# Kernel tuning notes

Hardware: AMD Instinct MI355X
Metric: run time of the kernel (lower is better)

## Reference

```python
import math
import jax, jax.numpy as jnp
import numpy as np

D_MODEL = 96
D_INNER = 192   # ssm_ratio * d_model
D_STATE = 16
DT_RANK = 6     # ceil(96/16)
B_, L_ = 4, 4096
LN_EPS = 1e-5


def selective_scan(u, delta, A, Bm, Cm, D):
    """Mamba selective scan (selective_scan_fn_v1 semantics).
    u, delta: [b,d,l]; A: [d,n]; Bm, Cm: [b,n,l]; D: [d]. Returns [b,d,l]."""
    b, d, l = u.shape
    n = A.shape[1]
    dT = jnp.transpose(delta, (2, 0, 1))  # [l,b,d]
    uT = jnp.transpose(u, (2, 0, 1))      # [l,b,d]
    BT = jnp.transpose(Bm, (2, 0, 1))     # [l,b,n]
    CT = jnp.transpose(Cm, (2, 0, 1))     # [l,b,n]

    def step(h, xs):
        dt, ut, Bt, Ct = xs
        dA = jnp.exp(dt[:, :, None] * A[None, :, :])            # [b,d,n]
        h = dA * h + (dt * ut)[:, :, None] * Bt[:, None, :]     # [b,d,n]
        y = jnp.sum(h * Ct[:, None, :], axis=-1)                # [b,d]
        return h, y

    h0 = jnp.zeros((b, d, n), u.dtype)
    _, ys = jax.lax.scan(step, h0, (dT, uT, BT, CT))            # ys: [l,b,d]
    return jnp.transpose(ys, (1, 2, 0)) + D[:, None] * u


def layer_norm(x, g, b):
    mu = jnp.mean(x, axis=-1, keepdims=True)
    var = jnp.var(x, axis=-1, keepdims=True)
    return (x - mu) * jax.lax.rsqrt(var + LN_EPS) * g + b


def branch_proj(x_bld, Wx, Wdt, bdt):
    """x_bld: [b,l,d_inner] -> delta [b,d,l], B [b,n,l], C [b,n,l]."""
    x_dbl = jnp.einsum('bld,kd->blk', x_bld, Wx)                # [b,l,r+2n]
    dt_r = x_dbl[..., :DT_RANK]
    Bm = jnp.transpose(x_dbl[..., DT_RANK:DT_RANK + D_STATE], (0, 2, 1))
    Cm = jnp.transpose(x_dbl[..., DT_RANK + D_STATE:], (0, 2, 1))
    dt = jnp.einsum('blr,dr->bdl', dt_r, Wdt)                   # [b,d,l]
    delta = jax.nn.softplus(dt + bdt[None, :, None])
    return delta, Bm, Cm


def forward_impl(x_rgb, x_share_rgb, x_e, x_share_e,
                 Wx1, Wx2, Wxs, Wdt1, Wdt2, Wdts, bdt1, bdt2, bdts,
                 Alog1, Alog2, Alogs, D1, D2, Ds,
                 g1, be1, g2, be2, gs, bes):
    u_rgb = jnp.transpose(x_rgb, (0, 2, 1))     # [b,d,l]
    u_e = jnp.transpose(x_e, (0, 2, 1))
    x_share = x_share_rgb + x_share_e           # [b,l,d]

    d_rgb, B_rgb, C_rgb = branch_proj(x_rgb, Wx1, Wdt1, bdt1)
    d_e, B_e, C_e = branch_proj(x_e, Wx2, Wdt2, bdt2)
    d_sh, B_sh, C_sh = branch_proj(x_share, Wxs, Wdts, bdts)

    A1 = -jnp.exp(Alog1)
    A2 = -jnp.exp(Alog2)
    As = -jnp.exp(Alogs)

    # Cross=True: rgb branch uses C from e branch, and vice versa
    y_rgb = selective_scan(u_rgb, d_rgb, A1, B_rgb, C_e, D1)
    y_e = selective_scan(u_e, d_e, A2, B_e, C_rgb, D2)
    y_sh_rgb = selective_scan(u_rgb, d_sh, As, B_sh, C_sh, Ds)
    y_sh_e = selective_scan(u_e, d_sh, As, B_sh, C_sh, Ds)

    y_rgb = layer_norm(jnp.transpose(y_rgb, (0, 2, 1)), g1, be1)
    y_e = layer_norm(jnp.transpose(y_e, (0, 2, 1)), g2, be2)
    y_sh_rgb = layer_norm(jnp.transpose(y_sh_rgb, (0, 2, 1)), gs, bes)
    y_sh_e = layer_norm(jnp.transpose(y_sh_e, (0, 2, 1)), gs, bes)
    return (y_rgb, y_sh_rgb, y_e, y_sh_e)


def setup_inputs() -> dict:
    key = jax.random.key(0)
    ks = jax.random.split(key, 16)
    inp = {}
    inp['x_rgb'] = jax.random.normal(ks[0], (B_, L_, D_INNER), jnp.float32)
    inp['x_share_rgb'] = jax.random.normal(ks[1], (B_, L_, D_INNER), jnp.float32)
    inp['x_e'] = jax.random.normal(ks[2], (B_, L_, D_INNER), jnp.float32)
    inp['x_share_e'] = jax.random.normal(ks[3], (B_, L_, D_INNER), jnp.float32)

    kproj = DT_RANK + 2 * D_STATE
    std = 1.0 / math.sqrt(D_INNER)
    inp['Wx1'] = jax.random.uniform(ks[4], (kproj, D_INNER), jnp.float32, -std, std)
    inp['Wx2'] = jax.random.uniform(ks[5], (kproj, D_INNER), jnp.float32, -std, std)
    inp['Wxs'] = jax.random.uniform(ks[6], (kproj, D_INNER), jnp.float32, -std, std)

    dt_std = DT_RANK ** -0.5
    inp['Wdt1'] = jax.random.uniform(ks[7], (D_INNER, DT_RANK), jnp.float32, -dt_std, dt_std)
    inp['Wdt2'] = jax.random.uniform(ks[8], (D_INNER, DT_RANK), jnp.float32, -dt_std, dt_std)
    inp['Wdts'] = jax.random.uniform(ks[9], (D_INNER, DT_RANK), jnp.float32, -dt_std, dt_std)

    def dt_bias(k):
        dt = jnp.exp(jax.random.uniform(k, (D_INNER,)) * (math.log(0.1) - math.log(0.001)) + math.log(0.001))
        dt = jnp.clip(dt, 1e-4, None)
        return dt + jnp.log(-jnp.expm1(-dt))  # inverse softplus
    inp['bdt1'] = dt_bias(ks[10])
    inp['bdt2'] = dt_bias(ks[11])
    inp['bdts'] = dt_bias(ks[12])

    Alog = jnp.log(jnp.broadcast_to(jnp.arange(1, D_STATE + 1, dtype=jnp.float32), (D_INNER, D_STATE)))
    inp['Alog1'] = Alog; inp['Alog2'] = Alog; inp['Alogs'] = Alog
    inp['D1'] = jnp.ones((D_INNER,), jnp.float32)
    inp['D2'] = jnp.ones((D_INNER,), jnp.float32)
    inp['Ds'] = jnp.ones((D_INNER,), jnp.float32)
    for nm in ('g1', 'g2', 'gs'):
        inp[nm] = jnp.ones((D_INNER,), jnp.float32)
    for nm in ('be1', 'be2', 'bes'):
        inp[nm] = jnp.zeros((D_INNER,), jnp.float32)
    return inp


def reference(x_rgb, x_share_rgb, x_e, x_share_e,
              Wx1, Wx2, Wxs, Wdt1, Wdt2, Wdts, bdt1, bdt2, bdts,
              Alog1, Alog2, Alogs, D1, D2, Ds,
              g1, be1, g2, be2, gs, bes):
    return forward_impl(x_rgb, x_share_rgb, x_e, x_share_e,
                        Wx1, Wx2, Wxs, Wdt1, Wdt2, Wdts, bdt1, bdt2, bdts,
                        Alog1, Alog2, Alogs, D1, D2, Ds,
                        g1, be1, g2, be2, gs, bes)
```

## Files before the change

kernel.cpp:

```cpp
#include <hip/hip_runtime.h>

#define B_ 4
#define L_ 4096
#define D_ 192
#define N_ 16
#define K_ 38
#define BLD (B_*L_*D_)
#define LOG2E 1.44269504088896f

__device__ __forceinline__ float fexp2(float x){ return __builtin_amdgcn_exp2f(x); }

__device__ __forceinline__ float softplus_f(float z){
    return fmaxf(z, 0.f) + __logf(1.f + __expf(-fabsf(z)));
}

__global__ __launch_bounds__(256) void proj_kernel(
    const float* __restrict__ xr,  const float* __restrict__ xsr,
    const float* __restrict__ xe,  const float* __restrict__ xse,
    const float* __restrict__ Wx1, const float* __restrict__ Wx2,
    const float* __restrict__ Wxs, float* __restrict__ xdbl)
{
    __shared__ float4 Wl[K_ * 48];
    __shared__ float4 xs[24 * 64];

    int branch = blockIdx.x >> 8;
    int tile   = blockIdx.x & 255;
    int tid  = threadIdx.x;
    int lane = tid & 63;
    int wv   = tid >> 6;

    const float* W = (branch == 0 ? Wx1 : branch == 1 ? Wx2 : Wxs);
    const float4* Wg = (const float4*)W;
    #pragma unroll
    for (int i = 0; i < 8; i++){
        int idx = tid + i * 256;
        if (idx < K_ * 48) Wl[idx] = Wg[idx];
    }

    const float* xA;
    const float* xB = nullptr;
    if (branch == 0)      xA = xr;
    else if (branch == 1) xA = xe;
    else { xA = xsr; xB = xse; }

    int c0 = wv * 10;
    int ncols = (wv < 3) ? 10 : 8;

    float acc[10];
    #pragma unroll
    for (int j = 0; j < 10; j++) acc[j] = 0.f;

    #pragma unroll
    for (int p = 0; p < 2; p++){
        __syncthreads();
        #pragma unroll
        for (int i = 0; i < 6; i++){
            int f4 = i * 256 + tid;
            int r  = f4 / 24;
            int kl = f4 - r * 24;
            const float4* src = (const float4*)(xA + (size_t)(tile * 64 + r) * D_);
            float4 v = src[p * 24 + kl];
            if (branch == 2){
                const float4* srcb = (const float4*)(xB + (size_t)(tile * 64 + r) * D_);
                float4 t = srcb[p * 24 + kl];
                v.x += t.x; v.y += t.y; v.z += t.z; v.w += t.w;
            }
            xs[kl * 64 + ((r + kl) & 63)] = v;
        }
        __syncthreads();
        #pragma unroll 4
        for (int kl = 0; kl < 24; kl++){
            float4 xv = xs[kl * 64 + ((lane + kl) & 63)];
            int k4 = p * 24 + kl;
            #pragma unroll
            for (int j = 0; j < 10; j++){
                if (j < ncols){
                    float4 wv4 = Wl[(c0 + j) * 48 + k4];
                    acc[j] = fmaf(xv.x, wv4.x, fmaf(xv.y, wv4.y,
                             fmaf(xv.z, wv4.z, fmaf(xv.w, wv4.w, acc[j]))));
                }
            }
        }
    }

    int gr = branch * (B_ * L_) + tile * 64 + lane;
    float* o = xdbl + (size_t)gr * K_ + c0;
    #pragma unroll
    for (int j = 0; j < 10; j++)
        if (j < ncols) o[j] = acc[j];
}

template<int NCt>
__global__ __launch_bounds__(192) void passA_kernel(
    const float* __restrict__ xdbl,
    const float* __restrict__ xr, const float* __restrict__ xe,
    const float* __restrict__ Wdt1, const float* __restrict__ Wdt2, const float* __restrict__ Wdts,
    const float* __restrict__ bdt1, const float* __restrict__ bdt2, const float* __restrict__ bdts,
    const float* __restrict__ Alog1, const float* __restrict__ Alog2, const float* __restrict__ Alogs,
    float* __restrict__ Sbuf, float* __restrict__ dsum)
{
    constexpr int CHt = L_ / NCt;
    int blk = blockIdx.x;
    int job = blk / (B_ * NCt);
    int rem = blk - job * (B_ * NCt);
    int b = rem / NCt;
    int c = rem - b * NCt;
    int d = threadIdx.x;
    const bool shared = (job == 2);

    const float* Wdt  = job == 0 ? Wdt1  : job == 1 ? Wdt2  : Wdts;
    const float* bdtp = job == 0 ? bdt1  : job == 1 ? bdt2  : bdts;
    const float* Alog = job == 0 ? Alog1 : job == 1 ? Alog2 : Alogs;

    float w[6];
    #pragma unroll
    for (int r = 0; r < 6; r++) w[r] = Wdt[d * 6 + r];
    float bd = bdtp[d];
    float A2[N_];
    #pragma unroll
    for (int n = 0; n < N_; n++) A2[n] = -__expf(Alog[d * N_ + n]) * LOG2E;

    float h[N_], h2[N_];
    #pragma unroll
    for (int n = 0; n < N_; n++){ h[n] = 0.f; h2[n] = 0.f; }
    float ds = 0.f;

    const float* u1 = (job == 1) ? xe : xr;
    const float* row = xdbl + ((size_t)(job * B_ + b) * L_ + (size_t)c * CHt) * K_;
    size_t uoff = ((size_t)b * L_ + (size_t)c * CHt) * D_ + d;

    float cur[22];
    #pragma unroll
    for (int i = 0; i < 22; i++) cur[i] = row[i];
    float uv  = u1[uoff];
    float uv2 = shared ? xe[uoff] : 0.f;

    for (int s = 0; s < CHt; s++){
        float nxt[22];
        #pragma unroll
        for (int i = 0; i < 22; i++) nxt[i] = row[K_ + i];
        size_t uoff_n = uoff + (s + 1 < CHt ? (size_t)D_ : 0);
        float uv_n  = u1[uoff_n];
        float uv2_n = shared ? xe[uoff_n] : 0.f;

        float z = bd;
        #pragma unroll
        for (int r = 0; r < 6; r++) z = fmaf(cur[r], w[r], z);
        float delta = softplus_f(z);
        ds += delta;
        float du  = delta * uv;
        float du2 = delta * uv2;
        #pragma unroll
        for (int n = 0; n < N_; n++){
            float dA = fexp2(delta * A2[n]);
            float bn = cur[6 + n];
            h[n] = fmaf(dA, h[n], du * bn);
            if (shared) h2[n] = fmaf(dA, h2[n], du2 * bn);
        }
        row += K_;
        #pragma unroll
        for (int i = 0; i < 22; i++) cur[i] = nxt[i];
        uv = uv_n; uv2 = uv2_n; uoff = uoff_n;
    }

    int inst = shared ? 2 : job;
    size_t sidx = ((((size_t)inst * B_ + b) * NCt + c) * D_ + d) * N_;
    #pragma unroll
    for (int n = 0; n < N_; n += 4)
        *(float4*)(Sbuf + sidx + n) = make_float4(h[n], h[n+1], h[n+2], h[n+3]);
    if (shared){
        size_t sidx2 = ((((size_t)3 * B_ + b) * NCt + c) * D_ + d) * N_;
        #pragma unroll
        for (int n = 0; n < N_; n += 4)
            *(float4*)(Sbuf + sidx2 + n) = make_float4(h2[n], h2[n+1], h2[n+2], h2[n+3]);
    }
    dsum[((size_t)(job * B_ + b) * NCt + c) * D_ + d] = ds;
}

template<int NCt>
__global__ __launch_bounds__(256) void combine_kernel(
    float* __restrict__ Sbuf, const float* __restrict__ dsum,
    const float* __restrict__ Alog1, const float* __restrict__ Alog2, const float* __restrict__ Alogs)
{
    int tid = blockIdx.x * 256 + threadIdx.x;
    int inst = tid / (B_ * D_ * N_);
    int rem  = tid - inst * (B_ * D_ * N_);
    int b  = rem / (D_ * N_);
    int dn = rem - b * (D_ * N_);
    int d = dn >> 4;
    int n = dn & 15;
    int branch = inst < 2 ? inst : 2;
    const float* Alog = inst == 0 ? Alog1 : inst == 1 ? Alog2 : Alogs;
    float A2 = -__expf(Alog[d * N_ + n]) * LOG2E;

    float h = 0.f;
    size_t base  = (((size_t)inst * B_ + b) * NCt) * (D_ * N_) + dn;
    size_t dbase = (((size_t)branch * B_ + b) * NCt) * D_ + d;
    for (int c = 0; c < NCt; c++){
        size_t idx = base + (size_t)c * (D_ * N_);
        float S = Sbuf[idx];
        Sbuf[idx] = h;
        float dd = dsum[dbase + (size_t)c * D_];
        h = fmaf(fexp2(A2 * dd), h, S);
    }
}

template<int NCt>
__global__ __launch_bounds__(192) void passC_kernel(
    const float* __restrict__ xdbl,
    const float* __restrict__ xr, const float* __restrict__ xe,
    const float* __restrict__ Wdt1, const float* __restrict__ Wdt2, const float* __restrict__ Wdts,
    const float* __restrict__ bdt1, const float* __restrict__ bdt2, const float* __restrict__ bdts,
    const float* __restrict__ Alog1, const float* __restrict__ Alog2, const float* __restrict__ Alogs,
    const float* __restrict__ Dp1, const float* __restrict__ Dp2, const float* __restrict__ Dps,
    const float* __restrict__ hstart,
    float* __restrict__ out)
{
    constexpr int CHt = L_ / NCt;
    int blk = blockIdx.x;
    int job = blk / (B_ * NCt);
    int rem = blk - job * (B_ * NCt);
    int b = rem / NCt;
    int c = rem - b * NCt;
    int d = threadIdx.x;
    const bool shared = (job == 2);

    const float* Wdt  = job == 0 ? Wdt1  : job == 1 ? Wdt2  : Wdts;
    const float* bdtp = job == 0 ? bdt1  : job == 1 ? bdt2  : bdts;
    const float* Alog = job == 0 ? Alog1 : job == 1 ? Alog2 : Alogs;
    float Dv = (job == 0 ? Dp1 : job == 1 ? Dp2 : Dps)[d];

    float w[6];
    #pragma unroll
    for (int r = 0; r < 6; r++) w[r] = Wdt[d * 6 + r];
    float bd = bdtp[d];
    float A2[N_];
    #pragma unroll
    for (int n = 0; n < N_; n++) A2[n] = -__expf(Alog[d * N_ + n]) * LOG2E;

    int inst = shared ? 2 : job;
    size_t hidx = ((((size_t)inst * B_ + b) * NCt + c) * D_ + d) * N_;
    float h[N_], h2[N_];
    #pragma unroll
    for (int n = 0; n < N_; n++) h[n] = hstart[hidx + n];
    if (shared){
        size_t hidx2 = ((((size_t)3 * B_ + b) * NCt + c) * D_ + d) * N_;
        #pragma unroll
        for (int n = 0; n < N_; n++) h2[n] = hstart[hidx2 + n];
    } else {
        #pragma unroll
        for (int n = 0; n < N_; n++) h2[n] = 0.f;
    }

    int cbranch = job == 0 ? 1 : job == 1 ? 0 : 2;
    const float* row  = xdbl + ((size_t)(job * B_ + b) * L_ + (size_t)c * CHt) * K_;
    const float* crow = xdbl + ((size_t)(cbranch * B_ + b) * L_ + (size_t)c * CHt) * K_ + 22;
    size_t uoff = ((size_t)b * L_ + (size_t)c * CHt) * D_ + d;
    const float* u1 = (job == 1) ? xe : xr;
    size_t obase1 = job == 0 ? 0 : job == 1 ? (size_t)2 * BLD : (size_t)1 * BLD;

    float cur[22], curC[N_];
    #pragma unroll
    for (int i = 0; i < 22; i++) cur[i] = row[i];
    #pragma unroll
    for (int n = 0; n < N_; n++) curC[n] = crow[n];
    float uv  = u1[uoff];
    float uv2 = shared ? xe[uoff] : 0.f;

    for (int s = 0; s < CHt; s++){
        float nxt[22], nxtC[N_];
        #pragma unroll
        for (int i = 0; i < 22; i++) nxt[i] = row[K_ + i];
        #pragma unroll
        for (int n = 0; n < N_; n++) nxtC[n] = crow[K_ + n];
        size_t uoff_n = uoff + (s + 1 < CHt ? (size_t)D_ : 0);
        float uv_n  = u1[uoff_n];
        float uv2_n = shared ? xe[uoff_n] : 0.f;

        float z = bd;
        #pragma unroll
        for (int r = 0; r < 6; r++) z = fmaf(cur[r], w[r], z);
        float delta = softplus_f(z);
        float du  = delta * uv;
        float du2 = delta * uv2;
        float y = 0.f, y2 = 0.f;
        #pragma unroll
        for (int n = 0; n < N_; n++){
            float dA = fexp2(delta * A2[n]);
            float bn = cur[6 + n];
            float cn = curC[n];
            h[n] = fmaf(dA, h[n], du * bn);
            y = fmaf(h[n], cn, y);
            if (shared){
                h2[n] = fmaf(dA, h2[n], du2 * bn);
                y2 = fmaf(h2[n], cn, y2);
            }
        }
        out[obase1 + uoff] = fmaf(Dv, uv, y);
        if (shared) out[(size_t)3 * BLD + uoff] = fmaf(Dv, uv2, y2);

        row += K_; crow += K_;
        #pragma unroll
        for (int i = 0; i < 22; i++) cur[i] = nxt[i];
        #pragma unroll
        for (int n = 0; n < N_; n++) curC[n] = nxtC[n];
        uv = uv_n; uv2 = uv2_n; uoff = uoff_n;
    }
}

__global__ __launch_bounds__(256) void ln_kernel(
    float* __restrict__ out,
    const float* __restrict__ g1, const float* __restrict__ be1,
    const float* __restrict__ g2, const float* __restrict__ be2,
    const float* __restrict__ gs, const float* __restrict__ bes)
{
    int wave = threadIdx.x >> 6;
    int lane = threadIdx.x & 63;
    int rowg = blockIdx.x * 4 + wave;
    int slot = rowg >> 14;
    size_t base = (size_t)rowg * D_;
    const float* g  = slot == 0 ? g1  : slot == 2 ? g2  : gs;
    const float* be = slot == 0 ? be1 : slot == 2 ? be2 : bes;
    float x0 = out[base + lane];
    float x1 = out[base + lane + 64];
    float x2 = out[base + lane + 128];
    float s = x0 + x1 + x2;
    float q = x0*x0 + x1*x1 + x2*x2;
    #pragma unroll
    for (int o = 32; o > 0; o >>= 1){
        s += __shfl_xor(s, o);
        q += __shfl_xor(q, o);
    }
    float mean = s * (1.f / 192.f);
    float var  = q * (1.f / 192.f) - mean * mean;
    float rs = rsqrtf(var + 1e-5f);
    out[base + lane]       = (x0 - mean) * rs * g[lane]       + be[lane];
    out[base + lane + 64]  = (x1 - mean) * rs * g[lane + 64]  + be[lane + 64];
    out[base + lane + 128] = (x2 - mean) * rs * g[lane + 128] + be[lane + 128];
}

extern "C" void kernel_launch(void* const* d_in, const int* in_sizes, int n_in,
                              void* d_out, int out_size, void* d_ws, size_t ws_size,
                              hipStream_t stream)
{
    const float* xr   = (const float*)d_in[0];
    const float* xsr  = (const float*)d_in[1];
    const float* xe   = (const float*)d_in[2];
    const float* xse  = (const float*)d_in[3];
    const float* Wx1  = (const float*)d_in[4];
    const float* Wx2  = (const float*)d_in[5];
    const float* Wxs  = (const float*)d_in[6];
    const float* Wdt1 = (const float*)d_in[7];
    const float* Wdt2 = (const float*)d_in[8];
    const float* Wdts = (const float*)d_in[9];
    const float* bdt1 = (const float*)d_in[10];
    const float* bdt2 = (const float*)d_in[11];
    const float* bdts = (const float*)d_in[12];
    const float* Alog1= (const float*)d_in[13];
    const float* Alog2= (const float*)d_in[14];
    const float* Alogs= (const float*)d_in[15];
    const float* Dp1  = (const float*)d_in[16];
    const float* Dp2  = (const float*)d_in[17];
    const float* Dps  = (const float*)d_in[18];
    const float* g1   = (const float*)d_in[19];
    const float* g2   = (const float*)d_in[20];
    const float* gs   = (const float*)d_in[21];
    const float* be1  = (const float*)d_in[22];
    const float* be2  = (const float*)d_in[23];
    const float* bes  = (const float*)d_in[24];

    float* ws = (float*)d_ws;
    float* out = (float*)d_out;

    const size_t xdbl_f = (size_t)3 * B_ * L_ * K_;
    const size_t need128 = (xdbl_f + (size_t)3*B_*128*D_ + (size_t)4*B_*128*D_*N_) * 4;

    proj_kernel<<<dim3(768), dim3(256), 0, stream>>>(xr, xsr, xe, xse, Wx1, Wx2, Wxs, ws);

    if (ws_size >= need128){
        constexpr int NCt = 128;
        float* xdbl = ws;
        float* dsum = xdbl + xdbl_f;
        float* Sbuf = dsum + (size_t)3 * B_ * NCt * D_;
        passA_kernel<NCt><<<dim3(3 * B_ * NCt), dim3(192), 0, stream>>>(xdbl, xr, xe,
            Wdt1, Wdt2, Wdts, bdt1, bdt2, bdts, Alog1, Alog2, Alogs, Sbuf, dsum);
        combine_kernel<NCt><<<dim3(192), dim3(256), 0, stream>>>(Sbuf, dsum, Alog1, Alog2, Alogs);
        passC_kernel<NCt><<<dim3(3 * B_ * NCt), dim3(192), 0, stream>>>(xdbl, xr, xe,
            Wdt1, Wdt2, Wdts, bdt1, bdt2, bdts, Alog1, Alog2, Alogs,
            Dp1, Dp2, Dps, Sbuf, out);
    } else {
        constexpr int NCt = 64;
        float* xdbl = ws;
        float* dsum = xdbl + xdbl_f;
        float* Sbuf = dsum + (size_t)3 * B_ * NCt * D_;
        passA_kernel<NCt><<<dim3(3 * B_ * NCt), dim3(192), 0, stream>>>(xdbl, xr, xe,
            Wdt1, Wdt2, Wdts, bdt1, bdt2, bdts, Alog1, Alog2, Alogs, Sbuf, dsum);
        combine_kernel<NCt><<<dim3(192), dim3(256), 0, stream>>>(Sbuf, dsum, Alog1, Alog2, Alogs);
        passC_kernel<NCt><<<dim3(3 * B_ * NCt), dim3(192), 0, stream>>>(xdbl, xr, xe,
            Wdt1, Wdt2, Wdts, bdt1, bdt2, bdts, Alog1, Alog2, Alogs,
            Dp1, Dp2, Dps, Sbuf, out);
    }

    ln_kernel<<<dim3(16384), dim3(256), 0, stream>>>(out, g1, be1, g2, be2, gs, bes);
}
```

Baseline: 297.5 us.

## Fuse LayerNorm into scan output pass via shared-memory row staging

Removes the separate LayerNorm kernel. The scan's output pass now stages 32 timesteps of y for all 192 channels in shared memory and normalizes each row with wave reductions before writing to global memory. It also reverses block order so the heavier shared-branch blocks launch first, splits the y reduction into four accumulators, and unrolls the time loops by 2. The aim is to avoid one full read and write of the output and a kernel launch, at the cost of more shared memory, barriers and register pressure in passC.

Measured after the change: 297.4 us. About the same (-0.0%).

```diff
diff --git a/kernel.cpp b/kernel.cpp
--- a/kernel.cpp
+++ b/kernel.cpp
@@ -101,8 +101,9 @@
 {
     constexpr int CHt = L_ / NCt;
     int blk = blockIdx.x;
-    int job = blk / (B_ * NCt);
-    int rem = blk - job * (B_ * NCt);
+    int q   = blk / (B_ * NCt);
+    int job = 2 - q;
+    int rem = blk - q * (B_ * NCt);
     int b = rem / NCt;
     int c = rem - b * NCt;
     int d = threadIdx.x;
@@ -135,6 +136,7 @@
     float uv  = u1[uoff];
     float uv2 = shared ? xe[uoff] : 0.f;
 
+    #pragma unroll 2
     for (int s = 0; s < CHt; s++){
         float nxt[22];
         #pragma unroll
@@ -213,22 +215,36 @@
     const float* __restrict__ bdt1, const float* __restrict__ bdt2, const float* __restrict__ bdts,
     const float* __restrict__ Alog1, const float* __restrict__ Alog2, const float* __restrict__ Alogs,
     const float* __restrict__ Dp1, const float* __restrict__ Dp2, const float* __restrict__ Dps,
+    const float* __restrict__ g1, const float* __restrict__ g2, const float* __restrict__ gs,
+    const float* __restrict__ be1, const float* __restrict__ be2, const float* __restrict__ bes,
     const float* __restrict__ hstart,
     float* __restrict__ out)
 {
     constexpr int CHt = L_ / NCt;
+    constexpr int NB  = CHt / 32;
+    __shared__ float ys [32 * D_];
+    __shared__ float ys2[32 * D_];
+
     int blk = blockIdx.x;
-    int job = blk / (B_ * NCt);
-    int rem = blk - job * (B_ * NCt);
+    int q   = blk / (B_ * NCt);
+    int job = 2 - q;
+    int rem = blk - q * (B_ * NCt);
     int b = rem / NCt;
     int c = rem - b * NCt;
     int d = threadIdx.x;
+    int lane = d & 63;
+    int wvi  = d >> 6;
     const bool shared = (job == 2);
 
     const float* Wdt  = job == 0 ? Wdt1  : job == 1 ? Wdt2  : Wdts;
     const float* bdtp = job == 0 ? bdt1  : job == 1 ? bdt2  : bdts;
     const float* Alog = job == 0 ? Alog1 : job == 1 ? Alog2 : Alogs;
     float Dv = (job == 0 ? Dp1 : job == 1 ? Dp2 : Dps)[d];
+    const float* gp = job == 0 ? g1  : job == 1 ? g2  : gs;
+    const float* bp = job == 0 ? be1 : job == 1 ? be2 : bes;
+    float gl[3], bl[3];
+    #pragma unroll
+    for (int i = 0; i < 3; i++){ gl[i] = gp[lane + 64*i]; bl[i] = bp[lane + 64*i]; }
 
     float w[6];
     #pragma unroll
@@ -267,76 +283,107 @@
     float uv  = u1[uoff];
     float uv2 = shared ? xe[uoff] : 0.f;
 
-    for (int s = 0; s < CHt; s++){
-        float nxt[22], nxtC[N_];
-        #pragma unroll
-        for (int i = 0; i < 22; i++) nxt[i] = row[K_ + i];
-        #pragma unroll
-        for (int n = 0; n < N_; n++) nxtC[n] = crow[K_ + n];
-        size_t uoff_n = uoff + (s + 1 < CHt ? (size_t)D_ : 0);
-        float uv_n  = u1[uoff_n];
-        float uv2_n = shared ? xe[uoff_n] : 0.f;
-
-        float z = bd;
-        #pragma unroll
-        for (int r = 0; r < 6; r++) z = fmaf(cur[r], w[r], z);
-        float delta = softplus_f(z);
-        float du  = delta * uv;
-        float du2 = delta * uv2;
-        float y = 0.f, y2 = 0.f;
-        #pragma unroll
-        for (int n = 0; n < N_; n++){
-            float dA = fexp2(delta * A2[n]);
-            float bn = cur[6 + n];
-            float cn = curC[n];
-            h[n] = fmaf(dA, h[n], du * bn);
-            y = fmaf(h[n], cn, y);
-            if (shared){
-                h2[n] = fmaf(dA, h2[n], du2 * bn);
-                y2 = fmaf(h2[n], cn, y2);
+    for (int batch = 0; batch < NB; batch++){
+        #pragma unroll 2
+        for (int t = 0; t < 32; t++){
+            int s = batch * 32 + t;
+            float nxt[22], nxtC[N_];
+            #pragma unroll
+            for (int i = 0; i < 22; i++) nxt[i] = row[K_ + i];
+            #pragma unroll
+            for (int n = 0; n < N_; n++) nxtC[n] = crow[K_ + n];
+            size_t uoff_n = uoff + (s + 1 < CHt ? (size_t)D_ : 0);
+            float uv_n  = u1[uoff_n];
+            float uv2_n = shared ? xe[uoff_n] : 0.f;
+
+            float z = bd;
+            #pragma unroll
+            for (int r = 0; r < 6; r++) z = fmaf(cur[r], w[r], z);
+            float delta = softplus_f(z);
+            float du  = delta * uv;
+            float du2 = delta * uv2;
+            float ya = 0.f, yb = 0.f, yc = 0.f, yd = 0.f;
+            float ya2 = 0.f, yb2 = 0.f, yc2 = 0.f, yd2 = 0.f;
+            #pragma unroll
+            for (int n = 0; n < N_; n += 4){
+                float dA0 = fexp2(delta * A2[n]);
+                float dA1 = fexp2(delta * A2[n+1]);
+                float dA2_ = fexp2(delta * A2[n+2]);
+                float dA3 = fexp2(delta * A2[n+3]);
+                h[n]   = fmaf(dA0, h[n],   du * cur[6+n]);
+                h[n+1] = fmaf(dA1, h[n+1], du * cur[7+n]);
+                h[n+2] = fmaf(dA2_, h[n+2], du * cur[8+n]);
+                h[n+3] = fmaf(dA3, h[n+3], du * cur[9+n]);
+                ya = fmaf(h[n],   curC[n],   ya);
+                yb = fmaf(h[n+1], curC[n+1], yb);
+                yc = fmaf(h[n+2], curC[n+2], yc);
+                yd = fmaf(h[n+3], curC[n+3], yd);
+                if (shared){
+                    h2[n]   = fmaf(dA0, h2[n],   du2 * cur[6+n]);
+                    h2[n+1] = fmaf(dA1, h2[n+1], du2 * cur[7+n]);
+                    h2[n+2] = fmaf(dA2_, h2[n+2], du2 * cur[8+n]);
+                    h2[n+3] = fmaf(dA3, h2[n+3], du2 * cur[9+n]);
+                    ya2 = fmaf(h2[n],   curC[n],   ya2);
+                    yb2 = fmaf(h2[n+1], curC[n+1], yb2);
+                    yc2 = fmaf(h2[n+2], curC[n+2], yc2);
+                    yd2 = fmaf(h2[n+3], curC[n+3], yd2);
+                }
             }
-        }
-        out[obase1 + uoff] = fmaf(Dv, uv, y);
-        if (shared) out[(size_t)3 * BLD + uoff] = fmaf(Dv, uv2, y2);
-
-        row += K_; crow += K_;
-        #pragma unroll
-        for (int i = 0; i < 22; i++) cur[i] = nxt[i];
-        #pragma unroll
-        for (int n = 0; n < N_; n++) curC[n] = nxtC[n];
-        uv = uv_n; uv2 = uv2_n; uoff = uoff_n;
-    }
-}
-
-__global__ __launch_bounds__(256) void ln_kernel(
-    float* __restrict__ out,
-    const float* __restrict__ g1, const float* __restrict__ be1,
-    const float* __restrict__ g2, const float* __restrict__ be2,
-    const float* __restrict__ gs, const float* __restrict__ bes)
-{
-    int wave = threadIdx.x >> 6;
-    int lane = threadIdx.x & 63;
-    int rowg = blockIdx.x * 4 + wave;
-    int slot = rowg >> 14;
-    size_t base = (size_t)rowg * D_;
-    const float* g  = slot == 0 ? g1  : slot == 2 ? g2  : gs;
-    const float* be = slot == 0 ? be1 : slot == 2 ? be2 : bes;
-    float x0 = out[base + lane];
-    float x1 = out[base + lane + 64];
-    float x2 = out[base + lane + 128];
-    float s = x0 + x1 + x2;
-    float q = x0*x0 + x1*x1 + x2*x2;
-    #pragma unroll
-    for (int o = 32; o > 0; o >>= 1){
-        s += __shfl_xor(s, o);
-        q += __shfl_xor(q, o);
-    }
-    float mean = s * (1.f / 192.f);
-    float var  = q * (1.f / 192.f) - mean * mean;
-    float rs = rsqrtf(var + 1e-5f);
-    out[base + lane]       = (x0 - mean) * rs * g[lane]       + be[lane];
-    out[base + lane + 64]  = (x1 - mean) * rs * g[lane + 64]  + be[lane + 64];
-    out[base + lane + 128] = (x2 - mean) * rs * g[lane + 128] + be[lane + 128];
+            ys[t * D_ + d] = fmaf(Dv, uv, (ya + yb) + (yc + yd));
+            if (shared) ys2[t * D_ + d] = fmaf(Dv, uv2, (ya2 + yb2) + (yc2 + yd2));
+
+            row += K_; crow += K_;
+            #pragma unroll
+            for (int i = 0; i < 22; i++) cur[i] = nxt[i];
+            #pragma unroll
+            for (int n = 0; n < N_; n++) curC[n] = nxtC[n];
+            uv = uv_n; uv2 = uv2_n; uoff = uoff_n;
+        }
+
+        __syncthreads();
+        size_t lbase = (size_t)b * L_ + (size_t)c * CHt + batch * 32;
+        for (int r = wvi; r < 32; r += 3){
+            float x0 = ys[r * D_ + lane];
+            float x1 = ys[r * D_ + lane + 64];
+            float x2 = ys[r * D_ + lane + 128];
+            float sm = x0 + x1 + x2;
+            float qm = x0*x0 + x1*x1 + x2*x2;
+            #pragma unroll
+            for (int o = 32; o > 0; o >>= 1){
+                sm += __shfl_xor(sm, o);
+                qm += __shfl_xor(qm, o);
+            }
+            float mean = sm * (1.f / 192.f);
+            float var  = qm * (1.f / 192.f) - mean * mean;
+            float rs = rsqrtf(var + 1e-5f);
+            float* ob = out + obase1 + (lbase + r) * D_;
+            ob[lane]       = (x0 - mean) * rs * gl[0] + bl[0];
+            ob[lane + 64]  = (x1 - mean) * rs * gl[1] + bl[1];
+            ob[lane + 128] = (x2 - mean) * rs * gl[2] + bl[2];
+        }
+        if (shared){
+            for (int r = wvi; r < 32; r += 3){
+                float x0 = ys2[r * D_ + lane];
+                float x1 = ys2[r * D_ + lane + 64];
+                float x2 = ys2[r * D_ + lane + 128];
+                float sm = x0 + x1 + x2;
+                float qm = x0*x0 + x1*x1 + x2*x2;
+                #pragma unroll
+                for (int o = 32; o > 0; o >>= 1){
+                    sm += __shfl_xor(sm, o);
+                    qm += __shfl_xor(qm, o);
+                }
+                float mean = sm * (1.f / 192.f);
+                float var  = qm * (1.f / 192.f) - mean * mean;
+                float rs = rsqrtf(var + 1e-5f);
+                float* ob = out + (size_t)3 * BLD + (lbase + r) * D_;
+                ob[lane]       = (x0 - mean) * rs * gl[0] + bl[0];
+                ob[lane + 64]  = (x1 - mean) * rs * gl[1] + bl[1];
+                ob[lane + 128] = (x2 - mean) * rs * gl[2] + bl[2];
+            }
+        }
+        __syncthreads();
+    }
 }
 
 extern "C" void kernel_launch(void* const* d_in, const int* in_sizes, int n_in,
@@ -387,7 +434,7 @@
         combine_kernel<NCt><<<dim3(192), dim3(256), 0, stream>>>(Sbuf, dsum, Alog1, Alog2, Alogs);
         passC_kernel<NCt><<<dim3(3 * B_ * NCt), dim3(192), 0, stream>>>(xdbl, xr, xe,
             Wdt1, Wdt2, Wdts, bdt1, bdt2, bdts, Alog1, Alog2, Alogs,
-            Dp1, Dp2, Dps, Sbuf, out);
+            Dp1, Dp2, Dps, g1, g2, gs, be1, be2, bes, Sbuf, out);
     } else {
         constexpr int NCt = 64;
         float* xdbl = ws;
@@ -398,8 +445,6 @@
         combine_kernel<NCt><<<dim3(192), dim3(256), 0, stream>>>(Sbuf, dsum, Alog1, Alog2, Alogs);
         passC_kernel<NCt><<<dim3(3 * B_ * NCt), dim3(192), 0, stream>>>(xdbl, xr, xe,
             Wdt1, Wdt2, Wdts, bdt1, bdt2, bdts, Alog1, Alog2, Alogs,
-            Dp1, Dp2, Dps, Sbuf, out);
-    }
-
-    ln_kernel<<<dim3(16384), dim3(256), 0, stream>>>(out, g1, be1, g2, be2, gs, bes);
-}
+            Dp1, Dp2, Dps, g1, g2, gs, be1, be2, bes, Sbuf, out);
+    }
+}
```
